# Kernel optimization log

Measured on AMD Instinct MI355X. Metric: run time of the kernel, lower is better.

Reference implementation:

```python
import jax, jax.numpy as jnp
import numpy as np
from jax import lax

N_SIN = 3

def _bn(x, g, b, m, v, eps):
    sh = [1] * x.ndim; sh[1] = -1
    r = lambda t: t.reshape(sh)
    return (x - r(m)) / jnp.sqrt(r(v) + eps) * r(g) + r(b)

def _conv2d(x, w, b, padding):
    y = lax.conv_general_dilated(x, w, (1, 1), padding,
                                 dimension_numbers=('NCHW', 'OIHW', 'NCHW'))
    return y + b[None, :, None, None]

def _causal_conv1d(x, w, b):
    k = w.shape[-1]
    y = lax.conv_general_dilated(x, w, (1,), [(k - 1, 0)],
                                 dimension_numbers=('NCH', 'OIH', 'NCH'))
    return y + b[None, :, None]

def _se(x, w1, w2):
    y = x.mean(axis=2)                                   # [B,C] global avg pool
    y = jax.nn.sigmoid(jax.nn.relu(y @ w1.T) @ w2.T)
    return x * y[:, :, None]

def _kan(x, W1, W2, B1, B2):
    # x: [B,din]; per-edge tiny MLP: sin/cos embed -> linear -> silu -> linear
    omega = (2.0 ** jnp.arange(N_SIN)).astype(x.dtype)   # [n_sin]
    ox = x[..., None] * omega                            # [B,din,n_sin]
    feat = jnp.concatenate([x[..., None], jnp.sin(ox), jnp.cos(ox)], axis=-1)  # [B,din,7]
    h = jnp.einsum('bif,ijhf->bijh', feat, W1) + B1[None]  # [B,din,dout,h]
    h = jax.nn.silu(h)
    out = jnp.einsum('bijh,ijh->bij', h, W2[:, :, 0, :]) + B2[None, :, :, 0]
    return out.sum(axis=1)                               # [B,dout]

def _lstm(x, w_ih, w_hh, b_ih, b_hh):
    B, T, E = x.shape
    H = w_hh.shape[1]
    def step(carry, xt):
        h, c = carry
        g = xt @ w_ih.T + h @ w_hh.T + (b_ih + b_hh)
        i, f, gg, o = jnp.split(g, 4, axis=-1)           # torch gate order i,f,g,o
        c = jax.nn.sigmoid(f) * c + jax.nn.sigmoid(i) * jnp.tanh(gg)
        h = jax.nn.sigmoid(o) * jnp.tanh(c)
        return (h, c), h
    init = (jnp.zeros((B, H), x.dtype), jnp.zeros((B, H), x.dtype))
    _, hs = lax.scan(step, init, jnp.swapaxes(x, 0, 1))
    return jnp.swapaxes(hs, 0, 1)                        # [B,T,H]

def _cluster(hidden):
    B, T, H = hidden.shape
    last = hidden[:, -1, :]
    hn = hidden / jnp.maximum(jnp.linalg.norm(hidden, axis=-1, keepdims=True), 1e-8)
    sim = jnp.einsum('bth,bsh->bts', hn, hn)
    sim = jnp.exp(-5.5 * (1.0 - sim))
    sim = sim * (1.0 - jnp.eye(T, dtype=sim.dtype))      # zero diagonal
    # 2-D prefix sums replace the O(T) python loop over block means
    S = jnp.cumsum(jnp.cumsum(sim, axis=1), axis=2)
    Sii = jnp.diagonal(S, axis1=1, axis2=2)[:, :T - 1]   # sum of [:i,:i]
    R = S[:, -1, :T - 1]                                 # sum of [:, :i]
    C = S[:, :T - 1, -1]                                 # sum of [:i, :]
    tot = S[:, -1, -1][:, None]
    i_f = jnp.arange(1, T, dtype=sim.dtype)
    dist = (Sii / i_f**2
            + (tot - R - C + Sii) / (T - i_f)**2
            - (C - Sii) / (i_f * (T - i_f))
            - (R - Sii) / (i_f * (T - i_f)))             # [B,T-1]
    cuts = jnp.argmax(dist, axis=1) + 1                  # [B]
    mask = (jnp.arange(T)[None, :] < cuts[:, None]).astype(hidden.dtype)
    corr = (hidden * mask[:, :, None]).sum(axis=1) / cuts[:, None].astype(hidden.dtype)
    return last, corr

def reference(x, we1, be1, bn_e1_g, bn_e1_b, bn_e1_m, bn_e1_v, we2, be2, bn_e2_g, bn_e2_b, bn_e2_m, bn_e2_v, w_ih, w_hh, b_ih, b_hh, mu_W1, mu_W2, mu_B1, mu_B2, std_W1, std_W2, std_B1, std_B2, muc_W1, muc_W2, muc_B1, muc_B2, stdc_W1, stdc_W2, stdc_B1, stdc_B2, fc_W1, fc_W2, fc_B1, fc_B2, wc1, bc1, bn1_g, bn1_b, bn1_m, bn1_v, se1_w1, se1_w2, wc2, bc2, bn2_g, bn2_b, bn2_m, bn2_v, se2_w1, se2_w2, wc3, bc3, bn3_g, bn3_b, bn3_m, bn3_v, eps1, eps2):
    gelu = lambda t: jax.nn.gelu(t, approximate=False)
    x = jnp.transpose(x, (0, 2, 1))                      # shuffle: [B,T,F]->[B,F,T]
    h2d = _conv2d(x[:, None], we1, be1, 'SAME')          # [B,4E,F,T]
    h2d = gelu(_bn(h2d, bn_e1_g, bn_e1_b, bn_e1_m, bn_e1_v, 1e-5))
    h2d = _conv2d(h2d, we2, be2, 'VALID')                # [B,E,1,T]
    h2d = gelu(_bn(h2d, bn_e2_g, bn_e2_b, bn_e2_m, bn_e2_v, 1e-5))
    x_src = jnp.transpose(h2d[:, :, 0, :], (0, 2, 1))    # [B,T,E]
    hseq = _lstm(x_src, w_ih, w_hh, b_ih, b_hh)          # [B,T,H]
    out, corr = _cluster(hseq)
    mu = _kan(corr, mu_W1, mu_W2, mu_B1, mu_B2)
    std = jax.nn.softplus(_kan(corr, std_W1, std_W2, std_B1, std_B2) - 5.0)
    z = mu + std * eps1
    x_z = jnp.concatenate([out, z], axis=1)              # [B,2H]
    mu_c = _kan(x_z, muc_W1, muc_W2, muc_B1, muc_B2)
    std_c = jax.nn.softplus(_kan(x_z, stdc_W1, stdc_W2, stdc_B1, stdc_B2) - 5.0)
    x1 = mu_c + std_c * eps2                             # dropout = identity (eval)
    x2 = jnp.transpose(x, (0, 2, 1))                     # [B,T,F]: channels = seq_len
    x2 = gelu(_bn(_causal_conv1d(x2, wc1, bc1), bn1_g, bn1_b, bn1_m, bn1_v, 1e-3))
    x2 = _se(x2, se1_w1, se1_w2)
    x2 = gelu(_bn(_causal_conv1d(x2, wc2, bc2), bn2_g, bn2_b, bn2_m, bn2_v, 1e-3))
    x2 = _se(x2, se2_w1, se2_w2)
    x2 = gelu(_bn(_causal_conv1d(x2, wc3, bc3), bn3_g, bn3_b, bn3_m, bn3_v, 1e-3))
    x2 = x2.mean(axis=2)                                 # [B,conv3_nf]
    x_all = jnp.concatenate([x1, x2], axis=1)            # [B, H+conv3_nf]
    return _kan(x_all, fc_W1, fc_W2, fc_B1, fc_B2)       # [B,num_classes]

def setup_inputs():
    key = jax.random.key(0)
    ks = iter(jax.random.split(key, 128))
    f32 = jnp.float32
    def n(shape, s=0.05):
        return s * jax.random.normal(next(ks), shape, f32)
    def bn_params(c):
        g = 1.0 + 0.05 * jax.random.normal(next(ks), (c,), f32)
        b = 0.05 * jax.random.normal(next(ks), (c,), f32)
        m = 0.05 * jax.random.normal(next(ks), (c,), f32)
        v = jax.random.uniform(next(ks), (c,), f32, 0.5, 1.5)
        return g, b, m, v
    def kan_params(din, dout, h=32, feat=1 + 2 * N_SIN):
        s = (2.0 / (feat + h)) ** 0.5
        return (n((din, dout, h, feat), s), n((din, dout, 1, h), s),
                jnp.zeros((din, dout, h), f32), jnp.zeros((din, dout, 1), f32))
    B, T, F_, E, H = 32, 256, 32, 64, 128
    inp = {}
    inp['x'] = jax.random.normal(next(ks), (B, T, F_), f32)
    inp['we1'] = n((4 * E, 1, 1, 8)); inp['be1'] = n((4 * E,))
    inp['bn_e1_g'], inp['bn_e1_b'], inp['bn_e1_m'], inp['bn_e1_v'] = bn_params(4 * E)
    inp['we2'] = n((E, 4 * E, F_, 1)); inp['be2'] = n((E,))
    inp['bn_e2_g'], inp['bn_e2_b'], inp['bn_e2_m'], inp['bn_e2_v'] = bn_params(E)
    inp['w_ih'] = n((4 * H, E)); inp['w_hh'] = n((4 * H, H))
    inp['b_ih'] = n((4 * H,)); inp['b_hh'] = n((4 * H,))
    for nm, (di, do) in [('mu', (H, H)), ('std', (H, H)), ('muc', (2 * H, H)), ('stdc', (2 * H, H)), ('fc', (2 * H, 10))]:
        w1, w2, b1, b2 = kan_params(di, do)
        inp[nm + '_W1'], inp[nm + '_W2'], inp[nm + '_B1'], inp[nm + '_B2'] = w1, w2, b1, b2
    inp['wc1'] = n((128, T, 8)); inp['bc1'] = n((128,))
    inp['bn1_g'], inp['bn1_b'], inp['bn1_m'], inp['bn1_v'] = bn_params(128)
    inp['se1_w1'] = n((8, 128)); inp['se1_w2'] = n((128, 8))
    inp['wc2'] = n((256, 128, 5)); inp['bc2'] = n((256,))
    inp['bn2_g'], inp['bn2_b'], inp['bn2_m'], inp['bn2_v'] = bn_params(256)
    inp['se2_w1'] = n((16, 256)); inp['se2_w2'] = n((256, 16))
    inp['wc3'] = n((128, 256, 3)); inp['bc3'] = n((128,))
    inp['bn3_g'], inp['bn3_b'], inp['bn3_m'], inp['bn3_v'] = bn_params(128)
    inp['eps1'] = jax.random.normal(next(ks), (B, H), f32)
    inp['eps2'] = jax.random.normal(next(ks), (B, H), f32)
    return inp
```

## Files before the change

### kernel.cpp

```cpp
#include <hip/hip_runtime.h>
#include <hip/hip_bf16.h>
#include <math.h>

typedef __hip_bfloat16 bf16;

#define DEV static __device__ __forceinline__

DEV float geluf(float x){ return 0.5f*x*(1.0f + erff(x*0.70710678118654752f)); }
DEV float sigmf(float x){ return 1.0f/(1.0f + __expf(-x)); }
DEV float softplusf(float x){ return (x > 15.f) ? x : log1pf(__expf(x)); }
DEV float tanhfast(float x){ float e = __expf(2.f*x); return fmaf(-2.f, 1.f/(e+1.f), 1.f); }

typedef __attribute__((ext_vector_type(8))) short v8s;
typedef __attribute__((ext_vector_type(4))) float v4f;
typedef _Float16 f16;
typedef f16 h2 __attribute__((ext_vector_type(2)));

DEV float dot2f(h2 a, h2 b, float c){
#if __has_builtin(__builtin_amdgcn_fdot2)
  return __builtin_amdgcn_fdot2(a, b, c, false);
#else
  return fmaf((float)a.y, (float)b.y, fmaf((float)a.x, (float)b.x, c));
#endif
}

enum : size_t {
  OFF_W1F   = 0,
  OFF_B1F   = 2048,
  OFF_S2E   = 2304,
  OFF_B2E   = 2368,
  OFF_WIHT  = 2432,
  OFF_BIASG = 35200,
  OFF_WHHT  = 35712,
  OFF_EPI1S = 101248,
  OFF_EPI1B = 101376,
  OFF_EPI2S = 101504,
  OFF_EPI2B = 101760,
  OFF_EPI3S = 102016,
  OFF_EPI3B = 102144,
  OFF_WE2B  = 102272,
  OFF_XSRC  = 364416,
  OFF_GX    = 888704,
  OFF_HSEQ  = 5083008,
  OFF_HN    = 6131584,
  OFF_PCOL  = 7180160,
  OFF_CCOL  = 7188352,
  OFF_CUTS  = 7196544,
  OFF_LAST  = 7196576,
  OFF_CORR  = 7200672,
  OFF_FEATA = 7204768,
  OFF_MUO   = 7233440,
  OFF_STDO  = 7237536,
  OFF_XZ    = 7241632,
  OFF_FEATB = 7249824,
  OFF_MUCO  = 7307168,
  OFF_STDCO = 7311264,
  OFF_XC1   = 7315360,
  OFF_XC2   = 7446432,
  OFF_KP    = 7708576,
  OFF_B2S   = 7741344,
  OFF_X2F   = 7839648,
  OFF_XALL  = 7843744,
  OFF_FEATC = 7851936,
  WS_FLOATS = 7909280
};

__global__ __launch_bounds__(256) void prep_kernel(
    const float* we1, const float* be1,
    const float* e1g, const float* e1b, const float* e1m, const float* e1v,
    const float* we2, const float* be2, const float* e2g, const float* e2b, const float* e2m, const float* e2v,
    const float* wih, const float* whh, const float* bih, const float* bhh,
    const float* bc1, const float* c1g, const float* c1b, const float* c1m, const float* c1v,
    const float* bc2, const float* c2g, const float* c2b, const float* c2m, const float* c2v,
    const float* bc3, const float* c3g, const float* c3b, const float* c3m, const float* c3v,
    const float* muB2, const float* sdB2, const float* mcB2, const float* scB2, const float* fcB2,
    float* ws)
{
  int idx = blockIdx.x*256 + threadIdx.x;
  if(idx < 2048){
    int o = idx>>3;
    float s = e1g[o] * rsqrtf(e1v[o] + 1e-5f);
    ws[OFF_W1F + idx] = we1[idx] * s;
  } else if(idx < 2304){
    int o = idx - 2048;
    float s = e1g[o] * rsqrtf(e1v[o] + 1e-5f);
    ws[OFF_B1F + o] = s*(be1[o] - e1m[o]) + e1b[o];
  } else if(idx < 2368){
    int e = idx - 2304;
    float s = e2g[e] * rsqrtf(e2v[e] + 1e-5f);
    ws[OFF_S2E + e] = s;
    ws[OFF_B2E + e] = s*(be2[e] - e2m[e]) + e2b[e];
  } else if(idx < 35136){
    int q = idx - 2368; int e = q>>9, g = q&511;
    ws[OFF_WIHT + q] = wih[g*64 + e];
  } else if(idx < 35648){
    int g = idx - 35136;
    ws[OFF_BIASG + g] = bih[g] + bhh[g];
  } else if(idx < 101184){
    int q = idx - 35648;
    if(q < 32768){
      int k2 = q>>9, g = q&511;
      h2 v;
      v.x = (f16)whh[g*128 + 2*k2];
      v.y = (f16)whh[g*128 + 2*k2 + 1];
      ((h2*)(ws + OFF_WHHT))[q] = v;
    }
  } else if(idx < 101312){
    int o = idx - 101184;
    float s = c1g[o] * rsqrtf(c1v[o] + 1e-3f);
    ws[OFF_EPI1S + o] = s;
    ws[OFF_EPI1B + o] = s*(bc1[o] - c1m[o]) + c1b[o];
  } else if(idx < 101568){
    int o = idx - 101312;
    float s = c2g[o] * rsqrtf(c2v[o] + 1e-3f);
    ws[OFF_EPI2S + o] = s;
    ws[OFF_EPI2B + o] = s*(bc2[o] - c2m[o]) + c2b[o];
  } else if(idx < 101696){
    int o = idx - 101568;
    float s = c3g[o] * rsqrtf(c3v[o] + 1e-3f);
    ws[OFF_EPI3S + o] = s;
    ws[OFF_EPI3B + o] = s*(bc3[o] - c3m[o]) + c3b[o];
  } else if(idx < 625984){
    int q = idx - 101696;
    int o = q >> 11, rem = q & 2047;
    int e = rem >> 5, f = rem & 31;
    bf16* Wr = (bf16*)(ws + OFF_WE2B);
    Wr[q] = __float2bfloat16(we2[(size_t)e*8192 + o*32 + f]);
  } else if(idx < 626112){
    int j = idx - 625984; float s = 0.f;
    for(int i=0;i<128;i++) s += muB2[i*128+j];
    ws[OFF_B2S + j] = s;
  } else if(idx < 626240){
    int j = idx - 626112; float s = 0.f;
    for(int i=0;i<128;i++) s += sdB2[i*128+j];
    ws[OFF_B2S + 128 + j] = s;
  } else if(idx < 626368){
    int j = idx - 626240; float s = 0.f;
    for(int i=0;i<256;i++) s += mcB2[i*128+j];
    ws[OFF_B2S + 256 + j] = s;
  } else if(idx < 626496){
    int j = idx - 626368; float s = 0.f;
    for(int i=0;i<256;i++) s += scB2[i*128+j];
    ws[OFF_B2S + 384 + j] = s;
  } else if(idx < 626506){
    int j = idx - 626496; float s = 0.f;
    for(int i=0;i<256;i++) s += fcB2[i*10+j];
    ws[OFF_B2S + 512 + j] = s;
  }
}

__global__ __launch_bounds__(256,1) void encoder_kernel(
    const float* __restrict__ x, const float* __restrict__ w1f, const float* __restrict__ b1f,
    const float* __restrict__ s2e, const float* __restrict__ b2e,
    const bf16* __restrict__ Wr, float* __restrict__ x_src)
{
  __shared__ float xs[39*32];
  __shared__ float w1s[2048];
  __shared__ float b1s[256];
  __shared__ __align__(16) unsigned short At[2][32*136];
  __shared__ __align__(16) unsigned short Bt[2][4*2560];

  int blk = blockIdx.x; int b = blk>>3; int t0 = (blk&7)*32;
  int tid = threadIdx.x;

  for(int i=tid;i<2048;i+=256) w1s[i] = w1f[i];
  b1s[tid] = b1f[tid];
  for(int i=tid;i<39*32;i+=256){
    int r=i>>5, f=i&31; int t=t0-3+r;
    xs[i] = (t>=0 && t<256) ? x[(b*256+t)*32+f] : 0.f;
  }
  __syncthreads();

  int f = tid & 31, tq = tid >> 5;
  int lane = tid & 63, w = tid >> 6;
  int wm = w & 1, wn = w >> 1;
  int m0 = wm*16, n0 = wn*32;
  int l15 = lane & 15, quad = lane >> 4;

  const v8s* Wv = (const v8s*)Wr;

  auto stage = [&](int cc, int buf){
    v8s bw[4];
    #pragma unroll
    for(int i=0;i<4;i++) bw[i] = Wv[cc*1024 + i*256 + tid];
    unsigned short aval[16];
    #pragma unroll
    for(int ol=0;ol<4;ol++){
      int o = cc*4 + ol;
      float wv[8];
      #pragma unroll
      for(int j=0;j<8;j++) wv[j] = w1s[o*8+j];
      float bb = b1s[o];
      #pragma unroll
      for(int i=0;i<4;i++){
        int tl = tq*4 + i;
        float c = bb;
        #pragma unroll
        for(int j=0;j<8;j++) c = fmaf(wv[j], xs[(tl+j)*32+f], c);
        aval[ol*4+i] = ((__hip_bfloat16_raw)__float2bfloat16(geluf(c))).x;
      }
    }
    #pragma unroll
    for(int ol=0;ol<4;ol++){
      #pragma unroll
      for(int i=0;i<4;i++)
        At[buf][(tq*4+i)*136 + ol*32 + f] = aval[ol*4+i];
    }
    #pragma unroll
    for(int i=0;i<4;i++){
      int j = i*256 + tid;
      int ol = j>>8, e = (j&255)>>2, f8 = j&3;
      *(v8s*)&Bt[buf][ol*2560 + e*40 + f8*8] = bw[i];
    }
  };

  stage(0, 0);
  __syncthreads();

  v4f acc0 = {0.f,0.f,0.f,0.f}, acc1 = {0.f,0.f,0.f,0.f};

  for(int c=0;c<64;c++){
    int p = c & 1, q = p ^ 1;
    if(c < 63) stage(c+1, q);
    #pragma unroll
    for(int ol=0;ol<4;ol++){
      v8s av = *(const v8s*)&At[p][(m0+l15)*136 + ol*32 + quad*8];
      v8s b0 = *(const v8s*)&Bt[p][ol*2560 + (n0+l15)*40 + quad*8];
      v8s b1 = *(const v8s*)&Bt[p][ol*2560 + (n0+16+l15)*40 + quad*8];
      acc0 = __builtin_amdgcn_mfma_f32_16x16x32_bf16(av, b0, acc0, 0, 0, 0);
      acc1 = __builtin_amdgcn_mfma_f32_16x16x32_bf16(av, b1, acc1, 0, 0, 0);
    }
    __syncthreads();
  }

  #pragma unroll
  for(int r=0;r<4;r++){
    int t = t0 + m0 + quad*4 + r;
    int e0 = n0 + l15;
    float v0 = geluf(s2e[e0]*acc0[r] + b2e[e0]);
    x_src[((size_t)(b*256+t))*64 + e0] = v0;
    int e1 = e0 + 16;
    float v1 = geluf(s2e[e1]*acc1[r] + b2e[e1]);
    x_src[((size_t)(b*256+t))*64 + e1] = v1;
  }
}

__global__ __launch_bounds__(256) void gates_kernel(
    const float* x_src, const float* wihT, const float* biasg, float* gx)
{
  __shared__ float xsh[32*64];
  int blk = blockIdx.x; int b = blk>>3, t0 = (blk&7)*32;
  int tid = threadIdx.x;
  for(int i=tid;i<2048;i+=256) xsh[i] = x_src[((size_t)b*256+t0)*64 + i];
  __syncthreads();
  int g0 = tid, g1 = tid + 256;
  float acc0[32], acc1[32];
  #pragma unroll
  for(int tt=0;tt<32;tt++){ acc0[tt]=0.f; acc1[tt]=0.f; }
  for(int e=0;e<64;e++){
    float w0 = wihT[e*512+g0], w1 = wihT[e*512+g1];
    #pragma unroll
    for(int tt=0;tt<32;tt++){
      float xv = xsh[tt*64+e];
      acc0[tt] = fmaf(xv, w0, acc0[tt]);
      acc1[tt] = fmaf(xv, w1, acc1[tt]);
    }
  }
  float bg0 = biasg[g0], bg1 = biasg[g1];
  #pragma unroll
  for(int tt=0;tt<32;tt++){
    gx[((size_t)b*256+t0+tt)*512 + g0] = acc0[tt] + bg0;
    gx[((size_t)b*256+t0+tt)*512 + g1] = acc1[tt] + bg1;
  }
}

__global__ __launch_bounds__(256,1) void lstm_kernel(
    const float* __restrict__ gates_x, const float* __restrict__ whh16f, float* __restrict__ hseq)
{
  __shared__ __align__(16) h2 hsh[2][64];
  __shared__ float fo_sh[256];
  int b = blockIdx.x, tt = threadIdx.x;
  const h2* W = (const h2*)whh16f;
  h2 w0[64], w1[64];
  #pragma unroll
  for(int k=0;k<64;k++){
    w0[k] = W[k*512 + tt];
    w1[k] = W[k*512 + 256 + tt];
  }
  int n = tt & 127;
  if(tt < 128) ((f16*)&hsh[0][0])[n] = (f16)0.f;
  float c = 0.f;
  const float* gx = gates_x + (size_t)b*256*512;
  float na0 = gx[tt], na1 = gx[256 + tt];
  __syncthreads();
  int p = 0;
  for(int t=0;t<256;t++){
    float a0 = na0, a1 = na1;
    if(t < 255){
      const float* gp = gx + (size_t)(t+1)*512;
      na0 = gp[tt]; na1 = gp[256 + tt];
    }
    #pragma unroll
    for(int kk=0;kk<64;kk++){
      h2 q = hsh[p][kk];
      a0 = dot2f(q, w0[kk], a0);
      a1 = dot2f(q, w1[kk], a1);
    }
    if(tt >= 128){
      fo_sh[n]       = a0;
      fo_sh[128 + n] = a1;
    }
    __syncthreads();
    if(tt < 128){
      float iv = sigmf(a0);
      float gv = tanhfast(a1);
      float fv = sigmf(fo_sh[n]);
      float ov = sigmf(fo_sh[128 + n]);
      c = fv*c + iv*gv;
      float h = ov*tanhfast(c);
      ((f16*)&hsh[p^1][0])[n] = (f16)h;
      hseq[((size_t)b*256+t)*128 + n] = h;
    }
    __syncthreads();
    p ^= 1;
  }
}

__global__ __launch_bounds__(64) void hn_kernel(const float* hseq, float* hn)
{
  size_t row = blockIdx.x; int lane = threadIdx.x;
  const float* hp = hseq + row*128;
  float v0 = hp[lane], v1 = hp[lane+64];
  float ss = v0*v0 + v1*v1;
  #pragma unroll
  for(int m=1;m<64;m<<=1) ss += __shfl_xor(ss, m, 64);
  float r = 1.f / fmaxf(sqrtf(ss), 1e-8f);
  hn[row*128 + lane]      = v0*r;
  hn[row*128 + 64 + lane] = v1*r;
}

__global__ __launch_bounds__(256) void pc_kernel(const float* hn, float* pcol, float* ccol)
{
  int blk = blockIdx.x; int b = blk>>3, chunk = blk&7;
  int tid = threadIdx.x; int il = tid & 31, ts = tid >> 5;
  int i = chunk*32 + il;
  const float4* hb = (const float4*)(hn + (size_t)b*32768);
  float4 hi[32];
  #pragma unroll
  for(int r=0;r<32;r++) hi[r] = hb[(size_t)i*32 + r];
  float ps=0.f, cs=0.f;
  for(int t=ts*32; t<ts*32+32; t++){
    float dx=0.f, dy=0.f, dz=0.f, dw=0.f;
    #pragma unroll
    for(int r=0;r<32;r++){
      float4 hv = hb[(size_t)t*32 + r];
      dx = fmaf(hi[r].x, hv.x, dx);
      dy = fmaf(hi[r].y, hv.y, dy);
      dz = fmaf(hi[r].z, hv.z, dz);
      dw = fmaf(hi[r].w, hv.w, dw);
    }
    float dot = (dx+dy)+(dz+dw);
    float sim = (t==i) ? 0.f : expf(-5.5f*(1.0f - dot));
    cs += sim;
    if(t < i) ps += sim;
  }
  __shared__ float red[16][32];
  red[ts][il] = ps; red[8+ts][il] = cs;
  __syncthreads();
  if(tid < 32){
    float s=0.f;
    for(int r=0;r<8;r++) s += red[r][tid];
    pcol[b*256 + chunk*32 + tid] = s;
  } else if(tid < 64){
    int c2 = tid - 32; float s=0.f;
    for(int r=0;r<8;r++) s += red[8+r][c2];
    ccol[b*256 + chunk*32 + c2] = s;
  }
}

__global__ __launch_bounds__(256) void cutcorr_kernel(
    const float* pcol, const float* ccol, const float* hseq,
    float* last, float* corr, int* cuts)
{
  int b = blockIdx.x, tid = threadIdx.x;
  __shared__ float D[256], RC[256], dist[256];
  __shared__ int cutsh;
  if(tid == 0){
    float d=0.f, r=0.f;
    for(int i=0;i<256;i++){
      d += 2.f*pcol[b*256+i]; D[i]=d;
      r += ccol[b*256+i];     RC[i]=r;
    }
  }
  __syncthreads();
  float tot = RC[255];
  if(tid < 255){
    float Dv = D[tid], Rv = RC[tid];
    float i_f = (float)(tid+1), j_f = 256.f - i_f;
    dist[tid] = Dv/(i_f*i_f) + (tot - 2.f*Rv + Dv)/(j_f*j_f) - 2.f*(Rv - Dv)/(i_f*j_f);
  }
  __syncthreads();
  if(tid == 0){
    float best = dist[0]; int bi = 0;
    for(int i=1;i<255;i++) if(dist[i] > best){ best = dist[i]; bi = i; }
    cutsh = bi + 1; cuts[b] = cutsh;
  }
  __syncthreads();
  int cut = cutsh;
  int k = tid & 127, half = tid >> 7;
  float s = 0.f;
  for(int t=half; t<cut; t+=2) s += hseq[((size_t)b*256+t)*128 + k];
  __shared__ float partial[2][128];
  partial[half][k] = s;
  __syncthreads();
  if(tid < 128){
    corr[b*128+tid] = (partial[0][tid] + partial[1][tid]) / (float)cut;
    last[b*128+tid] = hseq[((size_t)b*256+255)*128 + tid];
  }
}

__global__ __launch_bounds__(256) void feat_kernel(const float* xin, float* feat, int n)
{
  int idx = blockIdx.x*256 + threadIdx.x;
  if(idx >= n) return;
  float xv = xin[idx];
  float* fp = feat + (size_t)idx*7;
  fp[0]=xv;
  fp[1]=sinf(xv); fp[2]=sinf(2.f*xv); fp[3]=sinf(4.f*xv);
  fp[4]=cosf(xv); fp[5]=cosf(2.f*xv); fp[6]=cosf(4.f*xv);
}

__global__ __launch_bounds__(256) void kanp_kernel(
    const float* __restrict__ feat, const float* __restrict__ W1,
    const float* __restrict__ B1, const float* __restrict__ W2,
    int din, int dout, float* __restrict__ partial)
{
  __shared__ float feat_s[32*225];
  __shared__ float red[8][32];
  int j = blockIdx.x, ic = blockIdx.y;
  int i0 = ic*32;
  int tid = threadIdx.x;
  int b = tid & 31, hg = tid >> 5;
  for(int q=tid; q<1792; q+=256){
    int br = q/56, qq = q - br*56;
    float4 v = *(const float4*)(feat + ((size_t)br*din + i0)*7 + qq*4);
    float* d = &feat_s[br*225 + qq*4];
    d[0]=v.x; d[1]=v.y; d[2]=v.z; d[3]=v.w;
  }
  __syncthreads();
  float acc = 0.f;
  const float* fb = &feat_s[b*225];
  for(int ii=0; ii<32; ii++){
    int i = i0 + ii;
    size_t hbase = ((size_t)i*dout + j)*32 + hg*4;
    const float4* w1p = (const float4*)(W1 + ((size_t)i*dout + j)*224 + hg*28);
    float w1a[28];
    #pragma unroll
    for(int q=0;q<7;q++) *(float4*)&w1a[q*4] = w1p[q];
    float4 b1v = *(const float4*)(B1 + hbase);
    float4 w2v = *(const float4*)(W2 + hbase);
    float f[7];
    #pragma unroll
    for(int q=0;q<7;q++) f[q] = fb[ii*7+q];
    float b1a[4] = {b1v.x, b1v.y, b1v.z, b1v.w};
    float w2a[4] = {w2v.x, w2v.y, w2v.z, w2v.w};
    #pragma unroll
    for(int hh=0;hh<4;hh++){
      float hv = b1a[hh];
      #pragma unroll
      for(int q=0;q<7;q++) hv = fmaf(f[q], w1a[hh*7+q], hv);
      float sv = hv / (1.f + __expf(-hv));
      acc = fmaf(sv, w2a[hh], acc);
    }
  }
  red[hg][b] = acc;
  __syncthreads();
  if(tid < 32){
    float s = 0.f;
    #pragma unroll
    for(int q=0;q<8;q++) s += red[q][tid];
    partial[((size_t)ic*32 + tid)*dout + j] = s;
  }
}

__global__ __launch_bounds__(256) void kanr_kernel(
    const float* __restrict__ partial, const float* __restrict__ b2s,
    int NI, int dout, float* __restrict__ outp)
{
  int idx = blockIdx.x*256 + threadIdx.x;
  if(idx >= 32*dout) return;
  int b = idx / dout, j = idx - b*dout;
  float s = b2s[j];
  for(int ic=0; ic<NI; ic++) s += partial[((size_t)ic*32 + b)*dout + j];
  outp[idx] = s;
}

__global__ __launch_bounds__(256) void zmix_kernel(
    const float* muo, const float* stdo, const float* eps1, const float* last, float* xz)
{
  int idx = blockIdx.x*256 + threadIdx.x;
  if(idx >= 4096) return;
  int b = idx >> 7, k = idx & 127;
  float z = muo[idx] + softplusf(stdo[idx] - 5.f)*eps1[idx];
  xz[b*256 + k]       = last[idx];
  xz[b*256 + 128 + k] = z;
}

__global__ __launch_bounds__(256) void xall_kernel(
    const float* muco, const float* stdco, const float* eps2, const float* x2f, float* xa)
{
  int idx = blockIdx.x*256 + threadIdx.x;
  if(idx >= 4096) return;
  int b = idx >> 7, k = idx & 127;
  xa[b*256 + k]       = muco[idx] + softplusf(stdco[idx] - 5.f)*eps2[idx];
  xa[b*256 + 128 + k] = x2f[idx];
}

template<int CIN, int K, int COUT, int NCH, int LG>
__global__ __launch_bounds__(COUT*LG, 1) void convp_kernel(
    const float* __restrict__ xin, const float* __restrict__ w, float* __restrict__ part)
{
  constexpr int L = 32/LG;
  constexpr int CCH = CIN/NCH;
  __shared__ float xsh[CCH*32];
  int b = blockIdx.x, ch = blockIdx.y;
  int tid = threadIdx.x;
  for(int i=tid; i<CCH*32; i+=COUT*LG) xsh[i] = xin[((size_t)b*CIN + ch*CCH)*32 + i];
  __syncthreads();
  int o = tid / LG, lh = tid % LG;
  int l0 = lh*L;
  float acc[L];
  #pragma unroll
  for(int j=0;j<L;j++) acc[j]=0.f;
  const float* wrow = w + ((size_t)o*CIN + ch*CCH)*K;
  for(int c=0;c<CCH;c++){
    float wv[K];
    #pragma unroll
    for(int k=0;k<K;k++) wv[k] = wrow[c*K + k];
    float xr[L+K-1];
    #pragma unroll
    for(int i=0;i<L+K-1;i++){
      int li = l0 - (K-1) + i;
      xr[i] = (li>=0) ? xsh[c*32+li] : 0.f;
    }
    #pragma unroll
    for(int j=0;j<L;j++){
      #pragma unroll
      for(int k=0;k<K;k++) acc[j] = fmaf(xr[j+k], wv[k], acc[j]);
    }
  }
  float* pp = part + (((size_t)ch*32 + b)*COUT + o)*32 + l0;
  #pragma unroll
  for(int j=0;j<L;j++) pp[j] = acc[j];
}

template<int C, int R, int NP>
__global__ __launch_bounds__(C,1) void sef_kernel(
    const float* __restrict__ part, const float* __restrict__ epi_s, const float* __restrict__ epi_b,
    const float* __restrict__ w1, const float* __restrict__ w2, float* __restrict__ out)
{
  __shared__ float mean[C];
  __shared__ float y1[R];
  int b = blockIdx.x, c = threadIdx.x;
  float g[32];
  #pragma unroll
  for(int l=0;l<32;l++) g[l]=0.f;
  for(int p=0;p<NP;p++){
    const float* pp = part + (((size_t)p*32 + b)*C + c)*32;
    #pragma unroll
    for(int l=0;l<32;l++) g[l] += pp[l];
  }
  float s = epi_s[c], bb = epi_b[c];
  float m = 0.f;
  #pragma unroll
  for(int l=0;l<32;l++){ g[l] = geluf(s*g[l]+bb); m += g[l]; }
  mean[c] = m*(1.f/32.f);
  __syncthreads();
  if(c < R){
    float t=0.f;
    for(int k=0;k<C;k++) t = fmaf(mean[k], w1[c*C+k], t);
    y1[c] = fmaxf(t,0.f);
  }
  __syncthreads();
  float t=0.f;
  #pragma unroll
  for(int k=0;k<R;k++) t = fmaf(y1[k], w2[c*R+k], t);
  float sc = sigmf(t);
  float* op = out + ((size_t)b*C + c)*32;
  #pragma unroll
  for(int l=0;l<32;l++) op[l] = g[l]*sc;
}

__global__ __launch_bounds__(128,1) void mean3f_kernel(
    const float* __restrict__ part, const float* __restrict__ epi_s, const float* __restrict__ epi_b,
    float* __restrict__ x2f)
{
  int b = blockIdx.x, c = threadIdx.x;
  float g[32];
  #pragma unroll
  for(int l=0;l<32;l++) g[l]=0.f;
  for(int p=0;p<8;p++){
    const float* pp = part + (((size_t)p*32 + b)*128 + c)*32;
    #pragma unroll
    for(int l=0;l<32;l++) g[l] += pp[l];
  }
  float s = epi_s[c], bb = epi_b[c];
  float m = 0.f;
  #pragma unroll
  for(int l=0;l<32;l++) m += geluf(s*g[l]+bb);
  x2f[b*128 + c] = m*(1.f/32.f);
}

extern "C" void kernel_launch(void* const* d_in, const int* in_sizes, int n_in,
                              void* d_out, int out_size, void* d_ws, size_t ws_size,
                              hipStream_t stream)
{
  const float* x    = (const float*)d_in[0];
  const float* we1  = (const float*)d_in[1];
  const float* be1  = (const float*)d_in[2];
  const float* e1g  = (const float*)d_in[3];
  const float* e1b  = (const float*)d_in[4];
  const float* e1m  = (const float*)d_in[5];
  const float* e1v  = (const float*)d_in[6];
  const float* we2  = (const float*)d_in[7];
  const float* be2  = (const float*)d_in[8];
  const float* e2g  = (const float*)d_in[9];
  const float* e2b  = (const float*)d_in[10];
  const float* e2m  = (const float*)d_in[11];
  const float* e2v  = (const float*)d_in[12];
  const float* wih  = (const float*)d_in[13];
  const float* whh  = (const float*)d_in[14];
  const float* bih  = (const float*)d_in[15];
  const float* bhh  = (const float*)d_in[16];
  const float* muW1 = (const float*)d_in[17];
  const float* muW2 = (const float*)d_in[18];
  const float* muB1 = (const float*)d_in[19];
  const float* muB2 = (const float*)d_in[20];
  const float* sdW1 = (const float*)d_in[21];
  const float* sdW2 = (const float*)d_in[22];
  const float* sdB1 = (const float*)d_in[23];
  const float* sdB2 = (const float*)d_in[24];
  const float* mcW1 = (const float*)d_in[25];
  const float* mcW2 = (const float*)d_in[26];
  const float* mcB1 = (const float*)d_in[27];
  const float* mcB2 = (const float*)d_in[28];
  const float* scW1 = (const float*)d_in[29];
  const float* scW2 = (const float*)d_in[30];
  const float* scB1 = (const float*)d_in[31];
  const float* scB2 = (const float*)d_in[32];
  const float* fcW1 = (const float*)d_in[33];
  const float* fcW2 = (const float*)d_in[34];
  const float* fcB1 = (const float*)d_in[35];
  const float* fcB2 = (const float*)d_in[36];
  const float* wc1  = (const float*)d_in[37];
  const float* bc1  = (const float*)d_in[38];
  const float* c1g  = (const float*)d_in[39];
  const float* c1b  = (const float*)d_in[40];
  const float* c1m  = (const float*)d_in[41];
  const float* c1v  = (const float*)d_in[42];
  const float* se1w1= (const float*)d_in[43];
  const float* se1w2= (const float*)d_in[44];
  const float* wc2  = (const float*)d_in[45];
  const float* bc2  = (const float*)d_in[46];
  const float* c2g  = (const float*)d_in[47];
  const float* c2b  = (const float*)d_in[48];
  const float* c2m  = (const float*)d_in[49];
  const float* c2v  = (const float*)d_in[50];
  const float* se2w1= (const float*)d_in[51];
  const float* se2w2= (const float*)d_in[52];
  const float* wc3  = (const float*)d_in[53];
  const float* bc3  = (const float*)d_in[54];
  const float* c3g  = (const float*)d_in[55];
  const float* c3b  = (const float*)d_in[56];
  const float* c3m  = (const float*)d_in[57];
  const float* c3v  = (const float*)d_in[58];
  const float* eps1 = (const float*)d_in[59];
  const float* eps2 = (const float*)d_in[60];

  float* ws = (float*)d_ws;
  float* part = ws + OFF_GX;
  float* kp   = ws + OFF_KP;
  float* b2s  = ws + OFF_B2S;

  prep_kernel<<<2448, 256, 0, stream>>>(we1, be1, e1g,e1b,e1m,e1v,
      we2, be2,e2g,e2b,e2m,e2v, wih,whh,bih,bhh,
      bc1,c1g,c1b,c1m,c1v, bc2,c2g,c2b,c2m,c2v, bc3,c3g,c3b,c3m,c3v,
      muB2, sdB2, mcB2, scB2, fcB2, ws);

  encoder_kernel<<<256, 256, 0, stream>>>(x, ws+OFF_W1F, ws+OFF_B1F,
      ws+OFF_S2E, ws+OFF_B2E, (const bf16*)(ws+OFF_WE2B), ws+OFF_XSRC);

  gates_kernel<<<256, 256, 0, stream>>>(ws+OFF_XSRC, ws+OFF_WIHT, ws+OFF_BIASG, ws+OFF_GX);
  lstm_kernel<<<32, 256, 0, stream>>>(ws+OFF_GX, ws+OFF_WHHT, ws+OFF_HSEQ);

  hn_kernel<<<8192, 64, 0, stream>>>(ws+OFF_HSEQ, ws+OFF_HN);
  pc_kernel<<<256, 256, 0, stream>>>(ws+OFF_HN, ws+OFF_PCOL, ws+OFF_CCOL);
  cutcorr_kernel<<<32, 256, 0, stream>>>(ws+OFF_PCOL, ws+OFF_CCOL, ws+OFF_HSEQ,
      ws+OFF_LAST, ws+OFF_CORR, (int*)(ws+OFF_CUTS));

  feat_kernel<<<16, 256, 0, stream>>>(ws+OFF_CORR, ws+OFF_FEATA, 4096);
  kanp_kernel<<<dim3(128,4), 256, 0, stream>>>(ws+OFF_FEATA, muW1, muB1, muW2, 128, 128, kp);
  kanr_kernel<<<16, 256, 0, stream>>>(kp, b2s+0, 4, 128, ws+OFF_MUO);
  kanp_kernel<<<dim3(128,4), 256, 0, stream>>>(ws+OFF_FEATA, sdW1, sdB1, sdW2, 128, 128, kp);
  kanr_kernel<<<16, 256, 0, stream>>>(kp, b2s+128, 4, 128, ws+OFF_STDO);
  zmix_kernel<<<16, 256, 0, stream>>>(ws+OFF_MUO, ws+OFF_STDO, eps1, ws+OFF_LAST, ws+OFF_XZ);
  feat_kernel<<<32, 256, 0, stream>>>(ws+OFF_XZ, ws+OFF_FEATB, 8192);
  kanp_kernel<<<dim3(128,8), 256, 0, stream>>>(ws+OFF_FEATB, mcW1, mcB1, mcW2, 256, 128, kp);
  kanr_kernel<<<16, 256, 0, stream>>>(kp, b2s+256, 8, 128, ws+OFF_MUCO);
  kanp_kernel<<<dim3(128,8), 256, 0, stream>>>(ws+OFF_FEATB, scW1, scB1, scW2, 256, 128, kp);
  kanr_kernel<<<16, 256, 0, stream>>>(kp, b2s+384, 8, 128, ws+OFF_STDCO);

  convp_kernel<256,8,128,8,2><<<dim3(32,8), 256, 0, stream>>>(x, wc1, part);
  sef_kernel<128,8,8><<<32, 128, 0, stream>>>(part, ws+OFF_EPI1S, ws+OFF_EPI1B, se1w1, se1w2, ws+OFF_XC1);
  convp_kernel<128,5,256,4,1><<<dim3(32,4), 256, 0, stream>>>(ws+OFF_XC1, wc2, part);
  sef_kernel<256,16,4><<<32, 256, 0, stream>>>(part, ws+OFF_EPI2S, ws+OFF_EPI2B, se2w1, se2w2, ws+OFF_XC2);
  convp_kernel<256,3,128,8,2><<<dim3(32,8), 256, 0, stream>>>(ws+OFF_XC2, wc3, part);
  mean3f_kernel<<<32, 128, 0, stream>>>(part, ws+OFF_EPI3S, ws+OFF_EPI3B, ws+OFF_X2F);

  xall_kernel<<<16, 256, 0, stream>>>(ws+OFF_MUCO, ws+OFF_STDCO, eps2, ws+OFF_X2F, ws+OFF_XALL);
  feat_kernel<<<32, 256, 0, stream>>>(ws+OFF_XALL, ws+OFF_FEATC, 8192);
  kanp_kernel<<<dim3(10,8), 256, 0, stream>>>(ws+OFF_FEATC, fcW1, fcB1, fcW2, 256, 10, kp);
  kanr_kernel<<<2, 256, 0, stream>>>(kp, b2s+512, 8, 10, (float*)d_out);
}
```

Baseline: 983.9 us.

## Spread LSTM gates across 512 threads with vectorized hidden-state loads

```diff
diff --git a/kernel.cpp b/kernel.cpp
--- a/kernel.cpp
+++ b/kernel.cpp
@@ -15,6 +15,7 @@
 typedef __attribute__((ext_vector_type(4))) float v4f;
 typedef _Float16 f16;
 typedef f16 h2 __attribute__((ext_vector_type(2)));
+typedef f16 f16x8 __attribute__((ext_vector_type(8)));
 
 DEV float dot2f(h2 a, h2 b, float c){
 #if __has_builtin(__builtin_amdgcn_fdot2)
@@ -23,6 +24,8 @@
   return fmaf((float)a.y, (float)b.y, fmaf((float)a.x, (float)b.x, c));
 #endif
 }
+
+DEV h2 geth2(f16x8 v, int j){ h2 r; r.x = v[2*j]; r.y = v[2*j+1]; return r; }
 
 enum : size_t {
   OFF_W1F   = 0,
@@ -274,51 +277,53 @@
   }
 }
 
-__global__ __launch_bounds__(256,1) void lstm_kernel(
+__global__ __launch_bounds__(512,2) void lstm_kernel(
     const float* __restrict__ gates_x, const float* __restrict__ whh16f, float* __restrict__ hseq)
 {
-  __shared__ __align__(16) h2 hsh[2][64];
-  __shared__ float fo_sh[256];
+  __shared__ __align__(16) f16 hsh[2][128];
+  __shared__ float act_sh[384];
   int b = blockIdx.x, tt = threadIdx.x;
   const h2* W = (const h2*)whh16f;
-  h2 w0[64], w1[64];
+  h2 w[64];
   #pragma unroll
   for(int k=0;k<64;k++){
-    w0[k] = W[k*512 + tt];
-    w1[k] = W[k*512 + 256 + tt];
-  }
-  int n = tt & 127;
-  if(tt < 128) ((f16*)&hsh[0][0])[n] = (f16)0.f;
+    unsigned u = __builtin_bit_cast(unsigned, W[k*512 + tt]);
+    asm volatile("" : "+v"(u));
+    w[k] = __builtin_bit_cast(h2, u);
+  }
+  int n = tt & 127, grp = tt >> 7;
+  if(tt < 128) hsh[0][n] = (f16)0.f;
   float c = 0.f;
   const float* gx = gates_x + (size_t)b*256*512;
-  float na0 = gx[tt], na1 = gx[256 + tt];
+  float na = gx[tt];
   __syncthreads();
   int p = 0;
   for(int t=0;t<256;t++){
-    float a0 = na0, a1 = na1;
-    if(t < 255){
-      const float* gp = gx + (size_t)(t+1)*512;
-      na0 = gp[tt]; na1 = gp[256 + tt];
-    }
-    #pragma unroll
-    for(int kk=0;kk<64;kk++){
-      h2 q = hsh[p][kk];
-      a0 = dot2f(q, w0[kk], a0);
-      a1 = dot2f(q, w1[kk], a1);
-    }
-    if(tt >= 128){
-      fo_sh[n]       = a0;
-      fo_sh[128 + n] = a1;
-    }
+    float a = na;
+    f16x8 qv[16];
+    #pragma unroll
+    for(int k=0;k<16;k++) qv[k] = *(const f16x8*)&hsh[p][k*8];
+    if(t < 255) na = gx[(size_t)(t+1)*512 + tt];
+    float s0=0.f, s1=0.f, s2=0.f, s3=0.f;
+    #pragma unroll
+    for(int k=0;k<16;k++){
+      s0 = dot2f(geth2(qv[k],0), w[4*k+0], s0);
+      s1 = dot2f(geth2(qv[k],1), w[4*k+1], s1);
+      s2 = dot2f(geth2(qv[k],2), w[4*k+2], s2);
+      s3 = dot2f(geth2(qv[k],3), w[4*k+3], s3);
+    }
+    a += (s0+s1)+(s2+s3);
+    float iv = 0.f;
+    if(grp == 0)      iv = sigmf(a);
+    else if(grp == 1) act_sh[n]       = sigmf(a);
+    else if(grp == 2) act_sh[128 + n] = tanhfast(a);
+    else              act_sh[256 + n] = sigmf(a);
     __syncthreads();
-    if(tt < 128){
-      float iv = sigmf(a0);
-      float gv = tanhfast(a1);
-      float fv = sigmf(fo_sh[n]);
-      float ov = sigmf(fo_sh[128 + n]);
+    if(grp == 0){
+      float fv = act_sh[n], gv = act_sh[128 + n], ov = act_sh[256 + n];
       c = fv*c + iv*gv;
       float h = ov*tanhfast(c);
-      ((f16*)&hsh[p^1][0])[n] = (f16)h;
+      hsh[p^1][n] = (f16)h;
       hseq[((size_t)b*256+t)*128 + n] = h;
     }
     __syncthreads();
@@ -691,7 +696,7 @@
       ws+OFF_S2E, ws+OFF_B2E, (const bf16*)(ws+OFF_WE2B), ws+OFF_XSRC);
 
   gates_kernel<<<256, 256, 0, stream>>>(ws+OFF_XSRC, ws+OFF_WIHT, ws+OFF_BIASG, ws+OFF_GX);
-  lstm_kernel<<<32, 256, 0, stream>>>(ws+OFF_GX, ws+OFF_WHHT, ws+OFF_HSEQ);
+  lstm_kernel<<<32, 512, 0, stream>>>(ws+OFF_GX, ws+OFF_WHHT, ws+OFF_HSEQ);
 
   hn_kernel<<<8192, 64, 0, stream>>>(ws+OFF_HSEQ, ws+OFF_HN);
   pc_kernel<<<256, 256, 0, stream>>>(ws+OFF_HN, ws+OFF_PCOL, ws+OFF_CCOL);
```

Result: no change. 977.5 us (-0.6%).
